# Kernel optimization log

Hardware: AMD Instinct MI355X
Metric: run time of the kernel (lower is better)

The kernel has to match this reference:

```python
import jax, jax.numpy as jnp
import numpy as np

B, L_R, H = 8, 128, 512
CTX_LEN, STATE_NUM, ACT_NUM = 256, 32, 32
L_SRC = CTX_LEN + STATE_NUM + ACT_NUM
N_VOCAB = 32000
N_TOPIC = 4096


def setup_inputs() -> dict:
    key = jax.random.key(0)
    ks = jax.random.split(key, 9)
    return {
        "dec_out": jax.random.normal(ks[0], (B, L_R, H), jnp.float32),
        "src_hidden": jax.random.normal(ks[1], (B, L_SRC, H), jnp.float32),
        "W_gen": jax.random.normal(ks[2], (H, N_VOCAB), jnp.float32) * 0.02,
        "b_gen": jnp.zeros((N_VOCAB,), jnp.float32),
        "src_mask": jax.random.randint(ks[3], (B, 1, L_SRC), 0, 2, jnp.int32),
        "context": jax.random.randint(ks[4], (B, CTX_LEN), 0, N_VOCAB, jnp.int32),
        "tp": jax.random.randint(ks[5], (B, STATE_NUM), 0, N_TOPIC, jnp.int32),
        "action": jax.random.randint(ks[6], (B, ACT_NUM), 0, N_TOPIC, jnp.int32),
        "loc2glo": jax.random.randint(ks[7], (N_TOPIC,), 0, N_VOCAB, jnp.int32),
    }


def _scatter_vocab(prob, idx):
    # prob: [L_r, L_seg], idx: [L_seg] global-vocab ids -> [L_r, n_vocab]
    # duplicate indices accumulate, matching torch scatter_add / one-hot bmm
    return jnp.zeros((prob.shape[0], N_VOCAB), prob.dtype).at[:, idx].add(prob)


def reference(dec_out, src_hidden, W_gen, b_gen, src_mask, context, tp, action, loc2glo):
    # gen logits: [B, L_r, n_vocab]
    gen_logit = jnp.einsum("blh,hv->blv", dec_out, W_gen) + b_gen
    # copy logits over concatenated source: [B, L_r, L_src]
    copy_logit = jnp.einsum("blh,bsh->bls", dec_out, src_hidden)
    copy_logit = jnp.where(src_mask == 0, jnp.float32(-1e9), copy_logit)
    logits = jnp.concatenate([gen_logit, copy_logit], axis=-1)
    logits = logits * (H ** -0.5)  # op.scale_prj
    probs = jax.nn.softmax(logits, axis=-1)

    gen_prob = probs[:, :, :N_VOCAB]
    copy_ctx = probs[:, :, N_VOCAB:N_VOCAB + CTX_LEN]
    copy_tp = probs[:, :, N_VOCAB + CTX_LEN:N_VOCAB + CTX_LEN + STATE_NUM]
    copy_ar = probs[:, :, N_VOCAB + CTX_LEN + STATE_NUM:]

    scatter = jax.vmap(_scatter_vocab)
    ctx_prob = scatter(copy_ctx, context)                 # replaces one-hot bmm
    tp_prob = scatter(copy_tp, loc2glo[tp])               # scatter_add via loc2glo gather
    ar_prob = scatter(copy_ar, loc2glo[action])

    return gen_prob + ctx_prob + tp_prob + ar_prob
```

## Files before the change

### kernel.cpp

```cpp
#include <hip/hip_runtime.h>
#include <stdint.h>
#include <stddef.h>

#define NV    32000
#define HDIM  512
#define LSRC  320
#define MROWS 1024
#define SCALEF 0.044194173824159216f

typedef unsigned short u16;
typedef unsigned int   u32;
typedef __attribute__((ext_vector_type(8))) short short8;
typedef __attribute__((ext_vector_type(4))) float floatx4;

__device__ __forceinline__ u16 f2bf(float f) {
  u32 x = __float_as_uint(f);
  return (u16)((x + 0x7fffu + ((x >> 16) & 1u)) >> 16);
}

typedef __attribute__((address_space(1))) void gvoid;
typedef __attribute__((address_space(3))) void lvoid;
__device__ __forceinline__ void cp16(const u16* g, u16* l) {
  __builtin_amdgcn_global_load_lds((gvoid*)g, (lvoid*)l, 16, 0, 0);
}

__global__ __launch_bounds__(256) void k_convA(const float* __restrict__ dec,
                                               u16* __restrict__ Ab,
                                               float* __restrict__ rowSum) {
  if (blockIdx.x == 0) {
    ((float4*)rowSum)[threadIdx.x] = (float4){0.f, 0.f, 0.f, 0.f};
  }
  int t = blockIdx.x * 256 + threadIdx.x;
  int o = t * 8;
  int tile = o >> 12;
  int mt = tile >> 4, kt = tile & 15;
  int mi = (o & 4095) >> 5, ki = o & 31;
  const float* s = dec + (size_t)(mt * 128 + mi) * HDIM + kt * 32 + ki;
  float4 a = ((const float4*)s)[0];
  float4 b = ((const float4*)s)[1];
  union { u16 h[8]; uint4 v; } pk;
  pk.h[0] = f2bf(a.x); pk.h[1] = f2bf(a.y); pk.h[2] = f2bf(a.z); pk.h[3] = f2bf(a.w);
  pk.h[4] = f2bf(b.x); pk.h[5] = f2bf(b.y); pk.h[6] = f2bf(b.z); pk.h[7] = f2bf(b.w);
  *(uint4*)(Ab + o) = pk.v;
}

__global__ __launch_bounds__(256) void k_convW(const float* __restrict__ W,
                                               u16* __restrict__ Wb) {
  __shared__ u16 lds[128 * 36];
  int tileId = blockIdx.x;
  int nt = tileId >> 4, kt = tileId & 15;
  int t = threadIdx.x;
  const float* src = W + (size_t)kt * 32 * NV + (size_t)nt * 128;
#pragma unroll
  for (int i = 0; i < 4; ++i) {
    int f = t + 256 * i;
    int kin = f >> 5, n4 = f & 31;
    float4 v = *(const float4*)(src + (size_t)kin * NV + n4 * 4);
    int base = (n4 * 4) * 36 + kin;
    lds[base]       = f2bf(v.x);
    lds[base + 36]  = f2bf(v.y);
    lds[base + 72]  = f2bf(v.z);
    lds[base + 108] = f2bf(v.w);
  }
  __syncthreads();
  u16* dst = Wb + (size_t)tileId * 4096;
#pragma unroll
  for (int j = 0; j < 2; ++j) {
    int o = t * 8 + j * 2048;
    int ni = o >> 5, ki0 = o & 31;
    const u16* p = &lds[ni * 36 + ki0];
    uint2 x = *(const uint2*)p;
    uint2 y = *(const uint2*)(p + 4);
    uint4 v; v.x = x.x; v.y = x.y; v.z = y.x; v.w = y.y;
    *(uint4*)(dst + o) = v;
  }
}

__global__ __launch_bounds__(256) void k_convS(const float* __restrict__ srch,
                                               u16* __restrict__ Sb) {
  int t = blockIdx.x * 256 + threadIdx.x;
  int o = t * 8;
  int ki = o & 31;
  int ni = (o >> 5) & 127;
  int kt = (o >> 12) & 15;
  int r  = o >> 16;
  int tile = r % 3, b = r / 3;
  int s = tile * 128 + ni;
  uint4 v;
  if (s < LSRC) {
    const float* p = srch + ((size_t)b * LSRC + s) * HDIM + kt * 32 + ki;
    float4 a = ((const float4*)p)[0];
    float4 c = ((const float4*)p)[1];
    union { u16 h[8]; uint4 u; } pk;
    pk.h[0] = f2bf(a.x); pk.h[1] = f2bf(a.y); pk.h[2] = f2bf(a.z); pk.h[3] = f2bf(a.w);
    pk.h[4] = f2bf(c.x); pk.h[5] = f2bf(c.y); pk.h[6] = f2bf(c.z); pk.h[7] = f2bf(c.w);
    v = pk.u;
  } else {
    v = (uint4){0u, 0u, 0u, 0u};
  }
  *(uint4*)(Sb + o) = v;
}

__global__ __launch_bounds__(256) void k_gemm(const u16* __restrict__ Ab,
                                              const u16* __restrict__ Wb,
                                              const u16* __restrict__ Sb,
                                              const float* __restrict__ bgen,
                                              const int* __restrict__ mask,
                                              u16* __restrict__ wsE,
                                              float* __restrict__ wsCopy,
                                              float* __restrict__ rowSum) {
  __shared__ u16 As[2][4096];
  __shared__ u16 Bs[2][4096];
  int bid = blockIdx.x;
  int x = (bid >> 3) & 7;
  int y = ((bid >> 6) << 3) | (bid & 7);
  if (y >= 253) return;
  int t = threadIdx.x;
  int wid = t >> 6, lane = t & 63;
  int wm = wid >> 1, wn = wid & 1;
  int quad = lane >> 4, l16 = lane & 15;

  const u16* At = Ab + (size_t)x * (16 * 4096);
  const u16* Bt = (y < 250) ? (Wb + (size_t)y * (16 * 4096))
                            : (Sb + (size_t)(x * 3 + (y - 250)) * (16 * 4096));
  const u16* Ag0 = At + wid * 1024 + lane * 8;
  const u16* Bg0 = Bt + wid * 1024 + lane * 8;
  u16* Al0 = &As[0][wid * 1024];
  u16* Bl0 = &Bs[0][wid * 1024];

  floatx4 acc[4][4];
#pragma unroll
  for (int i = 0; i < 4; ++i)
#pragma unroll
    for (int j = 0; j < 4; ++j) acc[i][j] = (floatx4){0.f, 0.f, 0.f, 0.f};

  cp16(Ag0,        Al0);
  cp16(Ag0 + 512,  Al0 + 512);
  cp16(Bg0,        Bl0);
  cp16(Bg0 + 512,  Bl0 + 512);
  __syncthreads();

  int cb = 0;
#pragma unroll
  for (int kt = 0; kt < 16; ++kt) {
    int nb = cb ^ 1;
    if (kt < 15) {
      const u16* ag = Ag0 + (kt + 1) * 4096;
      const u16* bg = Bg0 + (kt + 1) * 4096;
      cp16(ag,       &As[nb][wid * 1024]);
      cp16(ag + 512, &As[nb][wid * 1024 + 512]);
      cp16(bg,       &Bs[nb][wid * 1024]);
      cp16(bg + 512, &Bs[nb][wid * 1024 + 512]);
    }
    short8 aR[4], bR[4];
#pragma unroll
    for (int mt = 0; mt < 4; ++mt)
      aR[mt] = *(const short8*)&As[cb][(wm * 64 + mt * 16 + l16) * 32 + quad * 8];
#pragma unroll
    for (int nt = 0; nt < 4; ++nt)
      bR[nt] = *(const short8*)&Bs[cb][(wn * 64 + nt * 16 + l16) * 32 + quad * 8];
#pragma unroll
    for (int mt = 0; mt < 4; ++mt)
#pragma unroll
      for (int nt = 0; nt < 4; ++nt)
        acc[mt][nt] = __builtin_amdgcn_mfma_f32_16x16x32_bf16(aR[mt], bR[nt],
                                                              acc[mt][nt], 0, 0, 0);
    __syncthreads();
    cb = nb;
  }

  int row0 = x * 128 + wm * 64;
  if (y < 250) {
    int col0 = y * 128 + wn * 64;
    float bg[4];
#pragma unroll
    for (int nt = 0; nt < 4; ++nt) bg[nt] = bgen[col0 + nt * 16 + l16];
#pragma unroll
    for (int mt = 0; mt < 4; ++mt) {
      float rs[4] = {0.f, 0.f, 0.f, 0.f};
#pragma unroll
      for (int nt = 0; nt < 4; ++nt) {
        int col = col0 + nt * 16 + l16;
#pragma unroll
        for (int r = 0; r < 4; ++r) {
          int row = row0 + mt * 16 + quad * 4 + r;
          float e = __expf((acc[mt][nt][r] + bg[nt]) * SCALEF);
          wsE[(size_t)row * NV + col] = f2bf(e);
          rs[r] += e;
        }
      }
#pragma unroll
      for (int r = 0; r < 4; ++r) {
        float v = rs[r];
        v += __shfl_xor(v, 1, 64);
        v += __shfl_xor(v, 2, 64);
        v += __shfl_xor(v, 4, 64);
        v += __shfl_xor(v, 8, 64);
        if (l16 == 0) atomicAdd(&rowSum[row0 + mt * 16 + quad * 4 + r], v);
      }
    }
  } else {
    int b = x;
    int sBase = (y - 250) * 128 + wn * 64;
#pragma unroll
    for (int mt = 0; mt < 4; ++mt) {
      float rs[4] = {0.f, 0.f, 0.f, 0.f};
#pragma unroll
      for (int nt = 0; nt < 4; ++nt) {
        int s = sBase + nt * 16 + l16;
        int valid = (s < LSRC);
        int m = valid ? mask[b * LSRC + s] : 0;
#pragma unroll
        for (int r = 0; r < 4; ++r) {
          int row = row0 + mt * 16 + quad * 4 + r;
          float e = m ? __expf(acc[mt][nt][r] * SCALEF) : 0.f;
          if (valid) wsCopy[row * LSRC + s] = e;
          rs[r] += e;
        }
      }
#pragma unroll
      for (int r = 0; r < 4; ++r) {
        float v = rs[r];
        v += __shfl_xor(v, 1, 64);
        v += __shfl_xor(v, 2, 64);
        v += __shfl_xor(v, 4, 64);
        v += __shfl_xor(v, 8, 64);
        if (l16 == 0) atomicAdd(&rowSum[row0 + mt * 16 + quad * 4 + r], v);
      }
    }
  }
}

__global__ __launch_bounds__(256) void k_norm(const u16* __restrict__ wsE,
                                              const float* __restrict__ wsCopy,
                                              const float* __restrict__ rowSum,
                                              const int* __restrict__ context,
                                              const int* __restrict__ tp,
                                              const int* __restrict__ action,
                                              const int* __restrict__ loc2glo,
                                              float* __restrict__ out) {
  int r = blockIdx.x, b = r >> 7;
  float inv = 1.0f / rowSum[r];
  const uint2* src = (const uint2*)(wsE + (size_t)r * NV);
  float4* dst = (float4*)(out + (size_t)r * NV);
  for (int c = threadIdx.x; c < NV / 4; c += 256) {
    uint2 v = src[c];
    float4 o;
    o.x = __uint_as_float(v.x << 16) * inv;
    o.y = __uint_as_float(v.x & 0xffff0000u) * inv;
    o.z = __uint_as_float(v.y << 16) * inv;
    o.w = __uint_as_float(v.y & 0xffff0000u) * inv;
    dst[c] = o;
  }
  __syncthreads();
  int t = threadIdx.x;
  float* op = out + (size_t)r * NV;
  atomicAdd(op + context[b * 256 + t], wsCopy[r * LSRC + t] * inv);
  if (t < 32) {
    atomicAdd(op + loc2glo[tp[b * 32 + t]],     wsCopy[r * LSRC + 256 + t] * inv);
    atomicAdd(op + loc2glo[action[b * 32 + t]], wsCopy[r * LSRC + 288 + t] * inv);
  }
}

extern "C" void kernel_launch(void* const* d_in, const int* in_sizes, int n_in,
                              void* d_out, int out_size, void* d_ws, size_t ws_size,
                              hipStream_t stream) {
  const float* dec  = (const float*)d_in[0];
  const float* srch = (const float*)d_in[1];
  const float* Wg   = (const float*)d_in[2];
  const float* bg   = (const float*)d_in[3];
  const int*   mask = (const int*)d_in[4];
  const int*   ctx  = (const int*)d_in[5];
  const int*   tp   = (const int*)d_in[6];
  const int*   act  = (const int*)d_in[7];
  const int*   l2g  = (const int*)d_in[8];
  float* out = (float*)d_out;

  char* ws = (char*)d_ws;
  u16*   Wb      = (u16*)(ws);
  u16*   wsE     = (u16*)(ws + 32768000);
  u16*   Ab      = (u16*)(ws + 98304000);
  float* wsCopy  = (float*)(ws + 99352576);
  float* rowSum  = (float*)(ws + 100663296);
  u16*   Sb      = (u16*)(ws + 100667392);

  hipLaunchKernelGGL(k_convA, dim3(256), dim3(256), 0, stream, dec, Ab, rowSum);
  hipLaunchKernelGGL(k_convW, dim3(4000), dim3(256), 0, stream, Wg, Wb);
  hipLaunchKernelGGL(k_convS, dim3(768), dim3(256), 0, stream, srch, Sb);
  hipLaunchKernelGGL(k_gemm, dim3(2048), dim3(256), 0, stream, Ab, Wb, Sb, bg, mask,
                     wsE, wsCopy, rowSum);
  hipLaunchKernelGGL(k_norm, dim3(MROWS), dim3(256), 0, stream, wsE, wsCopy, rowSum,
                     ctx, tp, act, l2g, out);
}
```

Before: 344.3 us.

## Use triple-buffered LDS with explicit vmcnt waits in GEMM main loop

Replaces the double-buffered async global-to-LDS pipeline with a three-stage ring buffer that prefetches two k-tiles ahead. Each iteration waits on vmcnt only for the oldest outstanding tile and issues a single barrier, instead of a full __syncthreads that drains all loads after every compute step. The aim is to hide more global-memory latency behind MFMA work. In exchange LDS use rises from 32KB to 48KB per block, which may lower occupancy, and correctness now depends on hand-counted vmcnt values.

Result: no change. 346.4 us (+0.6%).

```diff
diff --git a/kernel.cpp b/kernel.cpp
--- a/kernel.cpp
+++ b/kernel.cpp
@@ -109,8 +109,8 @@
                                               u16* __restrict__ wsE,
                                               float* __restrict__ wsCopy,
                                               float* __restrict__ rowSum) {
-  __shared__ u16 As[2][4096];
-  __shared__ u16 Bs[2][4096];
+  __shared__ u16 As[3][4096];
+  __shared__ u16 Bs[3][4096];
   int bid = blockIdx.x;
   int x = (bid >> 3) & 7;
   int y = ((bid >> 6) << 3) | (bid & 7);
@@ -125,8 +125,6 @@
                             : (Sb + (size_t)(x * 3 + (y - 250)) * (16 * 4096));
   const u16* Ag0 = At + wid * 1024 + lane * 8;
   const u16* Bg0 = Bt + wid * 1024 + lane * 8;
-  u16* Al0 = &As[0][wid * 1024];
-  u16* Bl0 = &Bs[0][wid * 1024];
 
   floatx4 acc[4][4];
 #pragma unroll
@@ -134,23 +132,32 @@
 #pragma unroll
     for (int j = 0; j < 4; ++j) acc[i][j] = (floatx4){0.f, 0.f, 0.f, 0.f};
 
-  cp16(Ag0,        Al0);
-  cp16(Ag0 + 512,  Al0 + 512);
-  cp16(Bg0,        Bl0);
-  cp16(Bg0 + 512,  Bl0 + 512);
-  __syncthreads();
-
-  int cb = 0;
+#pragma unroll
+  for (int p = 0; p < 2; ++p) {
+    const u16* ag = Ag0 + p * 4096;
+    const u16* bg = Bg0 + p * 4096;
+    cp16(ag,       &As[p][wid * 1024]);
+    cp16(ag + 512, &As[p][wid * 1024 + 512]);
+    cp16(bg,       &Bs[p][wid * 1024]);
+    cp16(bg + 512, &Bs[p][wid * 1024 + 512]);
+  }
+
 #pragma unroll
   for (int kt = 0; kt < 16; ++kt) {
-    int nb = cb ^ 1;
-    if (kt < 15) {
-      const u16* ag = Ag0 + (kt + 1) * 4096;
-      const u16* bg = Bg0 + (kt + 1) * 4096;
-      cp16(ag,       &As[nb][wid * 1024]);
-      cp16(ag + 512, &As[nb][wid * 1024 + 512]);
-      cp16(bg,       &Bs[nb][wid * 1024]);
-      cp16(bg + 512, &Bs[nb][wid * 1024 + 512]);
+    const int cb = kt % 3;
+    asm volatile("s_waitcnt lgkmcnt(0)" ::: "memory");
+    if (kt < 15) asm volatile("s_waitcnt vmcnt(4)" ::: "memory");
+    else         asm volatile("s_waitcnt vmcnt(0)" ::: "memory");
+    __builtin_amdgcn_s_barrier();
+    asm volatile("" ::: "memory");
+    if (kt < 14) {
+      const int sb = (kt + 2) % 3;
+      const u16* ag = Ag0 + (kt + 2) * 4096;
+      const u16* bg = Bg0 + (kt + 2) * 4096;
+      cp16(ag,       &As[sb][wid * 1024]);
+      cp16(ag + 512, &As[sb][wid * 1024 + 512]);
+      cp16(bg,       &Bs[sb][wid * 1024]);
+      cp16(bg + 512, &Bs[sb][wid * 1024 + 512]);
     }
     short8 aR[4], bR[4];
 #pragma unroll
@@ -165,8 +172,6 @@
       for (int nt = 0; nt < 4; ++nt)
         acc[mt][nt] = __builtin_amdgcn_mfma_f32_16x16x32_bf16(aR[mt], bR[nt],
                                                               acc[mt][nt], 0, 0, 0);
-    __syncthreads();
-    cb = nb;
   }
 
   int row0 = x * 128 + wm * 64;
```
